# Kernel optimization log

Hardware: AMD Instinct MI355X
Metric: run time of the kernel (lower is better)

Reference implementation:

```python
import jax, jax.numpy as jnp
import numpy as np

B, S, EMB = 2048, 512, 64
CARD = [2, 2, 2, 11, 19, 31, 34]  # gender, korean, primary, job, place, add, rep


def setup_inputs() -> dict:
    key = jax.random.key(0)
    ks = jax.random.split(key, 24)
    cont_x = jax.random.normal(ks[0], (B, S, 5), dtype=jnp.float32)
    cols = [jax.random.randint(ks[1 + i], (B, S, 1), 0, c) for i, c in enumerate(CARD)]
    cat_x = jnp.concatenate(cols, axis=2).astype(jnp.int32)  # [B,S,7]
    length = jax.random.randint(ks[8], (B,), 1, S + 1).astype(jnp.int32)  # valid lengths >= 1
    inp = {"cont_x": cont_x, "cat_x": cat_x, "length": length}
    for i, c in enumerate(CARD):
        inp[f"emb{i}"] = jax.random.normal(ks[9 + i], (c, EMB), dtype=jnp.float32) * 0.02
    inp["W_cont"] = jax.random.normal(ks[16], (5, EMB), dtype=jnp.float32) * (1.0 / np.sqrt(5.0))
    inp["b_cont"] = jnp.zeros((EMB,), dtype=jnp.float32)
    inp["W1"] = jax.random.normal(ks[17], (128, 64), dtype=jnp.float32) * (1.0 / np.sqrt(128.0))
    inp["b1"] = jnp.zeros((64,), dtype=jnp.float32)
    inp["W2"] = jax.random.normal(ks[18], (64, 2), dtype=jnp.float32) * (1.0 / np.sqrt(64.0))
    inp["b2"] = jnp.zeros((2,), dtype=jnp.float32)
    return inp


def reference(cont_x, cat_x, length, emb0, emb1, emb2, emb3, emb4, emb5, emb6,
              W_cont, b_cont, W1, b1, W2, b2):
    tables = (emb0, emb1, emb2, emb3, emb4, emb5, emb6)
    # mean of 7 per-column embedding lookups -> [B,S,EMB]
    cat_embs = sum(t[cat_x[:, :, i]] for i, t in enumerate(tables)) / 7.0
    cont_h = jax.nn.relu(cont_x @ W_cont + b_cont)  # [B,S,EMB]
    x = jnp.concatenate([cat_embs, cont_h], axis=2)  # [B,S,128]
    # fused masked segment-mean over valid prefix (replaces per-sample host loop)
    mask = (jnp.arange(x.shape[1])[None, :] < length[:, None]).astype(x.dtype)  # [B,S]
    pooled = jnp.einsum('bsd,bs->bd', x, mask) / length[:, None].astype(x.dtype)
    h = jax.nn.relu(pooled @ W1 + b1)
    out = jax.nn.relu(h @ W2 + b2)  # dropout p=0.0 -> identity
    return out
```

## Files before the change

### kernel.cpp

```cpp
#include <hip/hip_runtime.h>
#include <hip/hip_bf16.h>


#define CARD3 11
#define CARD4 19
#define CARD5 31
#define CARD6 34

typedef __attribute__((ext_vector_type(8))) short bf16x8;
typedef __attribute__((ext_vector_type(4))) float f32x4;
typedef __attribute__((ext_vector_type(4))) unsigned uintx4;
typedef int   int4a  __attribute__((ext_vector_type(4), aligned(4)));
typedef int   int2a  __attribute__((ext_vector_type(2), aligned(4)));
typedef float flt4a  __attribute__((ext_vector_type(4), aligned(4)));

static __device__ __forceinline__ unsigned pk_bf16(float a, float b) {
    unsigned ua = __float_as_uint(a), ub = __float_as_uint(b);
    ua += 0x7FFFu + ((ua >> 16) & 1u);
    ub += 0x7FFFu + ((ub >> 16) & 1u);
    return ((ua >> 16) & 0xFFFFu) | (ub & 0xFFFF0000u);
}

static __device__ __forceinline__ float rdlane(float v, int i) {
    return __builtin_bit_cast(float,
        __builtin_amdgcn_readlane(__builtin_bit_cast(int, v), i));
}

__global__ __launch_bounds__(64) void mlp_wave(
    const float* __restrict__ cont_x,
    const int*   __restrict__ cat_x,
    const int*   __restrict__ length,
    const float* __restrict__ e0, const float* __restrict__ e1,
    const float* __restrict__ e2, const float* __restrict__ e3,
    const float* __restrict__ e4, const float* __restrict__ e5,
    const float* __restrict__ e6,
    const float* __restrict__ W_cont,
    const float* __restrict__ b_cont,
    const float* __restrict__ W1,
    const float* __restrict__ b1,
    const float* __restrict__ W2,
    const float* __restrict__ b2,
    float*       __restrict__ out,
    int S)
{
    constexpr int HOFF[4] = {0, 11, 30, 61};
    constexpr int CARD[7] = {2, 2, 2, CARD3, CARD4, CARD5, CARD6};
    constexpr int OFFB[7] = {0, 2, 4, 6, 17, 36, 67};

    __shared__ int   hist[96];
    __shared__ float pcontl[64];

    const int b    = blockIdx.x;
    const int l    = threadIdx.x;
    const int lo16 = l & 15;
    const bool lo  = (l < 16);

    const int len = length[b];
    const int nt  = (len + 63) >> 6;

    hist[l] = 0;
    if (l < 32) hist[64 + l] = 0;

    const int*   cat7  = cat_x  + (size_t)b * S * 7;
    const float* cont5 = cont_x + (size_t)b * S * 5;

    unsigned q0, q1, q2;
    {
        const float w0 = W_cont[l],        w1 = W_cont[64 + l];
        const float w2 = W_cont[128 + l],  w3 = W_cont[192 + l];
        const float w4 = W_cont[256 + l],  w5 = b_cont[l];
        q0 = pk_bf16(w0, w1); q1 = pk_bf16(w2, w3); q2 = pk_bf16(w4, w5);
    }
    bf16x8 Bf[4];
#pragma unroll
    for (int ntc = 0; ntc < 4; ++ntc) {
        const int src = ntc * 16 + lo16;
        unsigned c0 = (unsigned)__shfl((int)q0, src);
        unsigned c1 = (unsigned)__shfl((int)q1, src);
        unsigned c2 = (unsigned)__shfl((int)q2, src);
        c0 = lo ? c0 : 0u; c1 = lo ? c1 : 0u; c2 = lo ? c2 : 0u;
        const uintx4 bu = {c0, c1, c2, 0u};
        Bf[ntc] = __builtin_bit_cast(bf16x8, bu);
    }

    int   c1pack = 0;
    f32x4 sum0 = {0.f, 0.f, 0.f, 0.f};
    f32x4 sum1 = sum0, sum2 = sum0, sum3 = sum0;
    const f32x4 z = {0.f, 0.f, 0.f, 0.f};

    int4a caA = {0,0,0,0}, caB = {0,0,0,0};
    int2a cbA = {0,0},     cbB = {0,0};
    int   ccA = 0,         ccB = 0;
    flt4a xaA = {0,0,0,0}, xaB = {0,0,0,0};
    float xbA = 0.f,       xbB = 0.f;

#define LOADA(T) do { const int* cp_ = cat7 + (size_t)((T)*64 + l) * 7;          \
        caA = *(const int4a*)cp_; cbA = *(const int2a*)(cp_ + 4); ccA = cp_[6];  \
        const float* xp_ = cont5 + (size_t)((T)*64 + l) * 5;                     \
        xaA = *(const flt4a*)xp_; xbA = xp_[4]; } while (0)
#define LOADB(T) do { const int* cp_ = cat7 + (size_t)((T)*64 + l) * 7;          \
        caB = *(const int4a*)cp_; cbB = *(const int2a*)(cp_ + 4); ccB = cp_[6];  \
        const float* xp_ = cont5 + (size_t)((T)*64 + l) * 5;                     \
        xaB = *(const flt4a*)xp_; xbB = xp_[4]; } while (0)

    auto COMPUTE = [&](int base, const int4a& ca, const int2a& cb, int cc,
                       const flt4a& xa, float xb) {
        const bool valid = (base + l < len);
        float x0 = 0.f, x1 = 0.f, x2 = 0.f, x3 = 0.f, x4 = 0.f;
        if (valid) {
            c1pack += ca.x + (ca.y << 10) + (ca.z << 20);
            atomicAdd(&hist[HOFF[0] + ca.w], 1);
            atomicAdd(&hist[HOFF[1] + cb.x], 1);
            atomicAdd(&hist[HOFF[2] + cb.y], 1);
            atomicAdd(&hist[HOFF[3] + cc],   1);
            x0 = xa.x; x1 = xa.y; x2 = xa.z; x3 = xa.w; x4 = xb;
        }
        const float aug = valid ? 1.0f : 0.0f;
        const unsigned p0 = pk_bf16(x0, x1);
        const unsigned p1 = pk_bf16(x2, x3);
        const unsigned p2 = pk_bf16(x4, aug);

#pragma unroll
        for (int t4 = 0; t4 < 4; ++t4) {
            const int src = t4 * 16 + lo16;
            unsigned a0 = (unsigned)__shfl((int)p0, src);
            unsigned a1 = (unsigned)__shfl((int)p1, src);
            unsigned a2 = (unsigned)__shfl((int)p2, src);
            a0 = lo ? a0 : 0u; a1 = lo ? a1 : 0u; a2 = lo ? a2 : 0u;
            const uintx4 au = {a0, a1, a2, 0u};
            const bf16x8 Af = __builtin_bit_cast(bf16x8, au);

            const f32x4 d0 = __builtin_amdgcn_mfma_f32_16x16x32_bf16(Af, Bf[0], z, 0, 0, 0);
            const f32x4 d1 = __builtin_amdgcn_mfma_f32_16x16x32_bf16(Af, Bf[1], z, 0, 0, 0);
            const f32x4 d2 = __builtin_amdgcn_mfma_f32_16x16x32_bf16(Af, Bf[2], z, 0, 0, 0);
            const f32x4 d3 = __builtin_amdgcn_mfma_f32_16x16x32_bf16(Af, Bf[3], z, 0, 0, 0);
#pragma unroll
            for (int i = 0; i < 4; ++i) {
                sum0[i] += fmaxf(d0[i], 0.f);
                sum1[i] += fmaxf(d1[i], 0.f);
                sum2[i] += fmaxf(d2[i], 0.f);
                sum3[i] += fmaxf(d3[i], 0.f);
            }
        }
    };

    LOADA(0);
    if (nt > 1) LOADB(1);
#pragma unroll 1
    for (int t = 0; t < nt; t += 2) {
        COMPUTE(t * 64, caA, cbA, ccA, xaA, xbA);
        if (t + 2 < nt) LOADA(t + 2);
        if (t + 1 < nt) {
            COMPUTE((t + 1) * 64, caB, cbB, ccB, xaB, xbB);
            if (t + 3 < nt) LOADB(t + 3);
        }
    }
#undef LOADA
#undef LOADB

#pragma unroll
    for (int off = 1; off <= 32; off <<= 1) c1pack += __shfl_xor(c1pack, off);

    float s0 = sum0[0] + sum0[1] + sum0[2] + sum0[3];
    float s1 = sum1[0] + sum1[1] + sum1[2] + sum1[3];
    float s2 = sum2[0] + sum2[1] + sum2[2] + sum2[3];
    float s3 = sum3[0] + sum3[1] + sum3[2] + sum3[3];
    s0 += __shfl_xor(s0, 16); s0 += __shfl_xor(s0, 32);
    s1 += __shfl_xor(s1, 16); s1 += __shfl_xor(s1, 32);
    s2 += __shfl_xor(s2, 16); s2 += __shfl_xor(s2, 32);
    s3 += __shfl_xor(s3, 16); s3 += __shfl_xor(s3, 32);
    if (lo) {
        pcontl[lo16]      = s0;
        pcontl[16 + lo16] = s1;
        pcontl[32 + lo16] = s2;
        pcontl[48 + lo16] = s3;
    }

    const float inv_len = 1.0f / (float)len;
    const float inv7    = inv_len * (1.0f / 7.0f);

    const float cmean = pcontl[l] * inv_len;

    float wA, wB;
    {
        const int j  = l >> 1;
        const int c1 = (c1pack >> (10 * j)) & 0x3FF;
        const float bw = (l & 1) ? (float)c1 : (float)(len - c1);
        wA = (l < 6) ? bw * inv7 : (float)hist[l - 6] * inv7;
        wB = (l < 37) ? (float)hist[58 + l] * inv7 : 0.f;
    }

    float pa0 = 0.f, pa1 = 0.f, pa2 = 0.f, pa3 = 0.f;
    {
        int cnt = 0;
#pragma unroll
        for (int t = 0; t < 7; ++t) {
            const float* tab = (t == 0) ? e0 : (t == 1) ? e1 : (t == 2) ? e2
                             : (t == 3) ? e3 : (t == 4) ? e4 : (t == 5) ? e5 : e6;
#pragma unroll
            for (int v = 0; v < CARD[t]; ++v) {
                const int i = OFFB[t] + v;
                const float f = (i < 64) ? rdlane(wA, i) : rdlane(wB, i - 64);
                const float ev = tab[v * 64 + l];
                if ((cnt & 3) == 0)      pa0 = fmaf(f, ev, pa0);
                else if ((cnt & 3) == 1) pa1 = fmaf(f, ev, pa1);
                else if ((cnt & 3) == 2) pa2 = fmaf(f, ev, pa2);
                else                     pa3 = fmaf(f, ev, pa3);
                ++cnt;
            }
        }
    }
    const float pcv = (pa0 + pa1) + (pa2 + pa3);

    float h0 = b1[l], h1 = 0.f, h2 = 0.f, h3 = 0.f;
#pragma unroll
    for (int d = 0; d < 64; ++d) {
        const float f = rdlane(pcv, d);
        const float wv = W1[d * 64 + l];
        if ((d & 3) == 0)      h0 = fmaf(f, wv, h0);
        else if ((d & 3) == 1) h1 = fmaf(f, wv, h1);
        else if ((d & 3) == 2) h2 = fmaf(f, wv, h2);
        else                   h3 = fmaf(f, wv, h3);
    }
#pragma unroll
    for (int d = 0; d < 64; ++d) {
        const float f = rdlane(cmean, d);
        const float wv = W1[(64 + d) * 64 + l];
        if ((d & 3) == 0)      h0 = fmaf(f, wv, h0);
        else if ((d & 3) == 1) h1 = fmaf(f, wv, h1);
        else if ((d & 3) == 2) h2 = fmaf(f, wv, h2);
        else                   h3 = fmaf(f, wv, h3);
    }
    const float h = fmaxf((h0 + h1) + (h2 + h3), 0.f);

    const float2 w2v = ((const float2*)W2)[l];
    float rr0 = h * w2v.x;
    float rr1 = h * w2v.y;
#pragma unroll
    for (int off = 1; off <= 32; off <<= 1) {
        rr0 += __shfl_xor(rr0, off);
        rr1 += __shfl_xor(rr1, off);
    }
    if (l == 0) {
        const float2 bb2 = *(const float2*)b2;
        float2 res;
        res.x = fmaxf(rr0 + bb2.x, 0.f);
        res.y = fmaxf(rr1 + bb2.y, 0.f);
        ((float2*)out)[b] = res;
    }
}

extern "C" void kernel_launch(void* const* d_in, const int* in_sizes, int n_in,
                              void* d_out, int out_size, void* d_ws, size_t ws_size,
                              hipStream_t stream)
{
    const float* cont_x = (const float*)d_in[0];
    const int*   cat_x  = (const int*)d_in[1];
    const int*   length = (const int*)d_in[2];
    const float* e0     = (const float*)d_in[3];
    const float* e1     = (const float*)d_in[4];
    const float* e2     = (const float*)d_in[5];
    const float* e3     = (const float*)d_in[6];
    const float* e4     = (const float*)d_in[7];
    const float* e5     = (const float*)d_in[8];
    const float* e6     = (const float*)d_in[9];
    const float* W_cont = (const float*)d_in[10];
    const float* b_cont = (const float*)d_in[11];
    const float* W1     = (const float*)d_in[12];
    const float* b1     = (const float*)d_in[13];
    const float* W2     = (const float*)d_in[14];
    const float* b2     = (const float*)d_in[15];
    float*       out    = (float*)d_out;

    const int B = in_sizes[2];
    const int S = in_sizes[0] / (B * 5);

    hipLaunchKernelGGL(mlp_wave, dim3(B), dim3(64), 0, stream,
                       cont_x, cat_x, length,
                       e0, e1, e2, e3, e4, e5, e6,
                       W_cont, b_cont, W1, b1, W2, b2,
                       out, S);
}
```

Before: 19.82 us.

## Split sequence tiles across two waves per block with shared-memory reduction

Each batch row is now handled by a 128-thread block in which two waves split the 64-row sequence tiles, taking even and odd tiles respectively. The loop is fully unrolled to at most four tiles per wave. Each wave keeps its own histogram, bit-packed counts and continuous-feature partial sums, and the first wave combines them after a barrier before running the MLP tail. This halves the serial per-row streaming latency and issues the first tile load earlier. In exchange it adds a block-wide sync and leaves the second wave idle during the tail. The unrolled loop assumes nt <= 8, i.e. S <= 512, which holds for this task.

```diff
diff --git a/kernel.cpp b/kernel.cpp
--- a/kernel.cpp
+++ b/kernel.cpp
@@ -26,7 +26,7 @@
         __builtin_amdgcn_readlane(__builtin_bit_cast(int, v), i));
 }
 
-__global__ __launch_bounds__(64) void mlp_wave(
+__global__ __launch_bounds__(128) void mlp_wave2(
     const float* __restrict__ cont_x,
     const int*   __restrict__ cat_x,
     const int*   __restrict__ length,
@@ -47,22 +47,44 @@
     constexpr int CARD[7] = {2, 2, 2, CARD3, CARD4, CARD5, CARD6};
     constexpr int OFFB[7] = {0, 2, 4, 6, 17, 36, 67};
 
-    __shared__ int   hist[96];
-    __shared__ float pcontl[64];
+    __shared__ int   hist[2][96];
+    __shared__ int   bc_s[2];
+    __shared__ float pcont[2][64];
 
     const int b    = blockIdx.x;
-    const int l    = threadIdx.x;
+    const int tid  = threadIdx.x;
+    const int wv   = tid >> 6;
+    const int l    = tid & 63;
     const int lo16 = l & 15;
     const bool lo  = (l < 16);
 
+    const int*   cat7  = cat_x  + (size_t)b * S * 7;
+    const float* cont5 = cont_x + (size_t)b * S * 5;
+
+    int4a caA = {0,0,0,0}, caB = {0,0,0,0};
+    int2a cbA = {0,0},     cbB = {0,0};
+    int   ccA = 0,         ccB = 0;
+    flt4a xaA = {0,0,0,0}, xaB = {0,0,0,0};
+    float xbA = 0.f,       xbB = 0.f;
+
+#define LOADA(T) do { const int* cp_ = cat7 + (size_t)((T)*64 + l) * 7;          \
+        caA = *(const int4a*)cp_; cbA = *(const int2a*)(cp_ + 4); ccA = cp_[6];  \
+        const float* xp_ = cont5 + (size_t)((T)*64 + l) * 5;                     \
+        xaA = *(const flt4a*)xp_; xbA = xp_[4]; } while (0)
+#define LOADB(T) do { const int* cp_ = cat7 + (size_t)((T)*64 + l) * 7;          \
+        caB = *(const int4a*)cp_; cbB = *(const int2a*)(cp_ + 4); ccB = cp_[6];  \
+        const float* xp_ = cont5 + (size_t)((T)*64 + l) * 5;                     \
+        xaB = *(const flt4a*)xp_; xbB = xp_[4]; } while (0)
+
+    const int t0 = wv;
+    LOADA(t0);
+
     const int len = length[b];
     const int nt  = (len + 63) >> 6;
-
-    hist[l] = 0;
-    if (l < 32) hist[64 + l] = 0;
-
-    const int*   cat7  = cat_x  + (size_t)b * S * 7;
-    const float* cont5 = cont_x + (size_t)b * S * 5;
+    const int t1  = wv + 2, t2 = wv + 4, t3 = wv + 6;
+
+    hist[wv][l] = 0;
+    if (l < 32) hist[wv][64 + l] = 0;
 
     unsigned q0, q1, q2;
     {
@@ -88,31 +110,16 @@
     f32x4 sum1 = sum0, sum2 = sum0, sum3 = sum0;
     const f32x4 z = {0.f, 0.f, 0.f, 0.f};
 
-    int4a caA = {0,0,0,0}, caB = {0,0,0,0};
-    int2a cbA = {0,0},     cbB = {0,0};
-    int   ccA = 0,         ccB = 0;
-    flt4a xaA = {0,0,0,0}, xaB = {0,0,0,0};
-    float xbA = 0.f,       xbB = 0.f;
-
-#define LOADA(T) do { const int* cp_ = cat7 + (size_t)((T)*64 + l) * 7;          \
-        caA = *(const int4a*)cp_; cbA = *(const int2a*)(cp_ + 4); ccA = cp_[6];  \
-        const float* xp_ = cont5 + (size_t)((T)*64 + l) * 5;                     \
-        xaA = *(const flt4a*)xp_; xbA = xp_[4]; } while (0)
-#define LOADB(T) do { const int* cp_ = cat7 + (size_t)((T)*64 + l) * 7;          \
-        caB = *(const int4a*)cp_; cbB = *(const int2a*)(cp_ + 4); ccB = cp_[6];  \
-        const float* xp_ = cont5 + (size_t)((T)*64 + l) * 5;                     \
-        xaB = *(const flt4a*)xp_; xbB = xp_[4]; } while (0)
-
     auto COMPUTE = [&](int base, const int4a& ca, const int2a& cb, int cc,
                        const flt4a& xa, float xb) {
         const bool valid = (base + l < len);
         float x0 = 0.f, x1 = 0.f, x2 = 0.f, x3 = 0.f, x4 = 0.f;
         if (valid) {
             c1pack += ca.x + (ca.y << 10) + (ca.z << 20);
-            atomicAdd(&hist[HOFF[0] + ca.w], 1);
-            atomicAdd(&hist[HOFF[1] + cb.x], 1);
-            atomicAdd(&hist[HOFF[2] + cb.y], 1);
-            atomicAdd(&hist[HOFF[3] + cc],   1);
+            atomicAdd(&hist[wv][HOFF[0] + ca.w], 1);
+            atomicAdd(&hist[wv][HOFF[1] + cb.x], 1);
+            atomicAdd(&hist[wv][HOFF[2] + cb.y], 1);
+            atomicAdd(&hist[wv][HOFF[3] + cc],   1);
             x0 = xa.x; x1 = xa.y; x2 = xa.z; x3 = xa.w; x4 = xb;
         }
         const float aug = valid ? 1.0f : 0.0f;
@@ -144,15 +151,17 @@
         }
     };
 
-    LOADA(0);
-    if (nt > 1) LOADB(1);
-#pragma unroll 1
-    for (int t = 0; t < nt; t += 2) {
-        COMPUTE(t * 64, caA, cbA, ccA, xaA, xbA);
-        if (t + 2 < nt) LOADA(t + 2);
-        if (t + 1 < nt) {
-            COMPUTE((t + 1) * 64, caB, cbB, ccB, xaB, xbB);
-            if (t + 3 < nt) LOADB(t + 3);
+    if (t0 < nt) {
+        if (t1 < nt) LOADB(t1);
+        COMPUTE(t0 * 64, caA, cbA, ccA, xaA, xbA);
+        if (t1 < nt) {
+            if (t2 < nt) LOADA(t2);
+            COMPUTE(t1 * 64, caB, cbB, ccB, xaB, xbB);
+            if (t2 < nt) {
+                if (t3 < nt) LOADB(t3);
+                COMPUTE(t2 * 64, caA, cbA, ccA, xaA, xbA);
+                if (t3 < nt) COMPUTE(t3 * 64, caB, cbB, ccB, xaB, xbB);
+            }
         }
     }
 #undef LOADA
@@ -160,6 +169,7 @@
 
 #pragma unroll
     for (int off = 1; off <= 32; off <<= 1) c1pack += __shfl_xor(c1pack, off);
+    if (l == 0) bc_s[wv] = c1pack;
 
     float s0 = sum0[0] + sum0[1] + sum0[2] + sum0[3];
     float s1 = sum1[0] + sum1[1] + sum1[2] + sum1[3];
@@ -170,24 +180,30 @@
     s2 += __shfl_xor(s2, 16); s2 += __shfl_xor(s2, 32);
     s3 += __shfl_xor(s3, 16); s3 += __shfl_xor(s3, 32);
     if (lo) {
-        pcontl[lo16]      = s0;
-        pcontl[16 + lo16] = s1;
-        pcontl[32 + lo16] = s2;
-        pcontl[48 + lo16] = s3;
-    }
+        pcont[wv][lo16]      = s0;
+        pcont[wv][16 + lo16] = s1;
+        pcont[wv][32 + lo16] = s2;
+        pcont[wv][48 + lo16] = s3;
+    }
+    __syncthreads();
+
+    if (tid >= 64) return;
 
     const float inv_len = 1.0f / (float)len;
     const float inv7    = inv_len * (1.0f / 7.0f);
 
-    const float cmean = pcontl[l] * inv_len;
+    const float cmean = (pcont[0][l] + pcont[1][l]) * inv_len;
+
+    const int c1pk = bc_s[0] + bc_s[1];
 
     float wA, wB;
     {
         const int j  = l >> 1;
-        const int c1 = (c1pack >> (10 * j)) & 0x3FF;
+        const int c1 = (c1pk >> (10 * j)) & 0x3FF;
         const float bw = (l & 1) ? (float)c1 : (float)(len - c1);
-        wA = (l < 6) ? bw * inv7 : (float)hist[l - 6] * inv7;
-        wB = (l < 37) ? (float)hist[58 + l] * inv7 : 0.f;
+        wA = (l < 6)  ? bw * inv7
+                      : (float)(hist[0][l - 6] + hist[1][l - 6]) * inv7;
+        wB = (l < 37) ? (float)(hist[0][58 + l] + hist[1][58 + l]) * inv7 : 0.f;
     }
 
     float pa0 = 0.f, pa1 = 0.f, pa2 = 0.f, pa3 = 0.f;
@@ -216,20 +232,20 @@
 #pragma unroll
     for (int d = 0; d < 64; ++d) {
         const float f = rdlane(pcv, d);
-        const float wv = W1[d * 64 + l];
-        if ((d & 3) == 0)      h0 = fmaf(f, wv, h0);
-        else if ((d & 3) == 1) h1 = fmaf(f, wv, h1);
-        else if ((d & 3) == 2) h2 = fmaf(f, wv, h2);
-        else                   h3 = fmaf(f, wv, h3);
+        const float wvv = W1[d * 64 + l];
+        if ((d & 3) == 0)      h0 = fmaf(f, wvv, h0);
+        else if ((d & 3) == 1) h1 = fmaf(f, wvv, h1);
+        else if ((d & 3) == 2) h2 = fmaf(f, wvv, h2);
+        else                   h3 = fmaf(f, wvv, h3);
     }
 #pragma unroll
     for (int d = 0; d < 64; ++d) {
         const float f = rdlane(cmean, d);
-        const float wv = W1[(64 + d) * 64 + l];
-        if ((d & 3) == 0)      h0 = fmaf(f, wv, h0);
-        else if ((d & 3) == 1) h1 = fmaf(f, wv, h1);
-        else if ((d & 3) == 2) h2 = fmaf(f, wv, h2);
-        else                   h3 = fmaf(f, wv, h3);
+        const float wvv = W1[(64 + d) * 64 + l];
+        if ((d & 3) == 0)      h0 = fmaf(f, wvv, h0);
+        else if ((d & 3) == 1) h1 = fmaf(f, wvv, h1);
+        else if ((d & 3) == 2) h2 = fmaf(f, wvv, h2);
+        else                   h3 = fmaf(f, wvv, h3);
     }
     const float h = fmaxf((h0 + h1) + (h2 + h3), 0.f);
 
@@ -275,7 +291,7 @@
     const int B = in_sizes[2];
     const int S = in_sizes[0] / (B * 5);
 
-    hipLaunchKernelGGL(mlp_wave, dim3(B), dim3(64), 0, stream,
+    hipLaunchKernelGGL(mlp_wave2, dim3(B), dim3(128), 0, stream,
                        cont_x, cat_x, length,
                        e0, e1, e2, e3, e4, e5, e6,
                        W_cont, b_cont, W1, b1, W2, b2,
```

New measurement: 20.76 us. 4.7% more time.
